# Performance work log

Hardware: AMD Instinct MI355X
Metric: run time of the kernel (lower is better)

## Reference

```python
import jax, jax.numpy as jnp
import numpy as np

B, N, F_IN = 8, 1024, 64
HEADS = 8
D = F_IN  # out_features per head (in_features == out_features)


def setup_inputs() -> dict:
    key = jax.random.key(0)
    ks = jax.random.split(key, 5)
    stdv = 1.0 / np.sqrt(F_IN * HEADS)
    h = jax.random.normal(ks[0], (B, N, F_IN), dtype=jnp.float32)
    adj = jnp.ones((B, N, N), dtype=jnp.float32)  # passed but unused by the module
    W = jax.random.uniform(ks[1], (F_IN, D * HEADS), minval=-stdv, maxval=stdv, dtype=jnp.float32)
    a = jax.random.uniform(ks[2], (2 * D, 1), minval=-stdv, maxval=stdv, dtype=jnp.float32)
    out_W = jax.random.normal(ks[3], (D * HEADS, F_IN), dtype=jnp.float32) / np.sqrt(D * HEADS)
    out_b = jnp.zeros((F_IN,), dtype=jnp.float32)
    return {"h": h, "adj": adj, "W": W, "a": a, "out_W": out_W, "out_b": out_b}


def reference(h, adj, W, a, out_W, out_b):
    Bv, Nv, _ = h.shape
    Dh = W.shape[1] // HEADS
    # Wh: [B, N, H, D]
    Wh = (h @ W).reshape(Bv, Nv, HEADS, Dh)
    # Additive attention decomposed: e[b,i,j,h] = leaky_relu(Wh[b,i,h].a_src + Wh[b,j,h].a_dst)
    a_src = jnp.einsum('bnhd,d->bnh', Wh, a[:Dh, 0])
    a_dst = jnp.einsum('bnhd,d->bnh', Wh, a[Dh:, 0])
    e = jax.nn.leaky_relu(a_src[:, :, None, :] + a_dst[:, None, :, :], negative_slope=0.01)  # [B,N,N,H]
    # Module applies softmax over dim=1 (the first node axis i)
    attn = jax.nn.softmax(e, axis=1)  # [B,N,N,H]
    # h_prime[b,i,h,:] = sum_j attn[b,i,j,h] * Wh[b,j,h,:]
    h_prime = jnp.einsum('bijh,bjhd->bihd', attn, Wh).reshape(Bv, Nv, HEADS * Dh)
    return h_prime @ out_W + out_b
```

## Files before the change

kernel.cpp:

```cpp
#include <hip/hip_runtime.h>


#define B_  8
#define N_  1024
#define H_  8
#define D_  64
#define BH_ 64
#define CH_ 32
#define CL_ 32

__device__ __forceinline__ float bcast_lane(float v, int l) {
  return __int_as_float(__builtin_amdgcn_readlane(__float_as_int(v), l));
}

__global__ __launch_bounds__(256) void k_wh(
    const float* __restrict__ h, const float* __restrict__ W,
    const float* __restrict__ a,
    float* __restrict__ Wh, float* __restrict__ sArr, float* __restrict__ tArr) {
  const int tid = threadIdx.x;
  const int lane = tid & 63;
  const int wid = tid >> 6;
  const int row0 = blockIdx.x * 16;
  const int b = row0 >> 10;

  float hreg[16];
#pragma unroll
  for (int r = 0; r < 16; ++r) hreg[r] = h[(row0 + r) * 64 + lane];
  const float a_s = a[lane];
  const float a_t = a[64 + lane];

  float acc0[16], acc1[16];
#pragma unroll
  for (int r = 0; r < 16; ++r) { acc0[r] = 0.f; acc1[r] = 0.f; }
#pragma unroll 4
  for (int k = 0; k < 64; ++k) {
    const float w0 = W[k * 512 + tid];
    const float w1 = W[k * 512 + tid + 256];
#pragma unroll
    for (int r = 0; r < 16; ++r) {
      const float hv = bcast_lane(hreg[r], k);
      acc0[r] += hv * w0;
      acc1[r] += hv * w1;
    }
  }
  const int hh0 = wid, hh1 = wid + 4;
#pragma unroll
  for (int r = 0; r < 16; ++r) {
    const int n = (row0 + r) & (N_ - 1);
    Wh[((b * H_ + hh0) * N_ + n) * D_ + lane] = acc0[r];
    Wh[((b * H_ + hh1) * N_ + n) * D_ + lane] = acc1[r];
  }
#pragma unroll
  for (int r = 0; r < 16; ++r) {
    const int n = (row0 + r) & (N_ - 1);
    float s0 = acc0[r] * a_s, t0 = acc0[r] * a_t;
    float s1 = acc1[r] * a_s, t1 = acc1[r] * a_t;
#pragma unroll
    for (int m = 32; m > 0; m >>= 1) {
      s0 += __shfl_xor(s0, m); t0 += __shfl_xor(t0, m);
      s1 += __shfl_xor(s1, m); t1 += __shfl_xor(t1, m);
    }
    if (lane == 0) {
      sArr[(b * H_ + hh0) * N_ + n] = s0;
      tArr[(b * H_ + hh0) * N_ + n] = t0;
      sArr[(b * H_ + hh1) * N_ + n] = s1;
      tArr[(b * H_ + hh1) * N_ + n] = t1;
    }
  }
}

__global__ __launch_bounds__(1024) void k_sortinc(
    const float* __restrict__ sArr, const float* __restrict__ tArr,
    const float* __restrict__ Wh,
    int* __restrict__ qrk,
    float* __restrict__ INC1, float* __restrict__ INC2,
    float2* __restrict__ cOff) {
  __shared__ float sL[1024];
  __shared__ float tvL[1024];
  __shared__ int   tiL[1024];
  __shared__ float cum1L[1024], cum001L[1024];
  __shared__ float2 cs12L[CH_ * 64];
  __shared__ float ws1[16], ws2[16];
  const int tid = threadIdx.x;
  const int lane = tid & 63;
  const int wv_ = tid >> 6;
  const int bh = blockIdx.x;

  const float orig_s = sArr[bh * N_ + tid];
  float sv_r = orig_s;
  float tv_r = tArr[bh * N_ + tid];
  int   ti_r = tid;

  for (int size = 2; size <= 1024; size <<= 1) {
    for (int stride = size >> 1; stride > 0; stride >>= 1) {
      const bool up = ((tid & size) == 0);
      const bool lower = ((tid & stride) == 0);
      float psv, ptv; int pti;
      if (stride >= 64) {
        sL[tid] = sv_r; tvL[tid] = tv_r; tiL[tid] = ti_r;
        __syncthreads();
        const int p = tid ^ stride;
        psv = sL[p]; ptv = tvL[p]; pti = tiL[p];
        __syncthreads();
      } else {
        psv = __shfl_xor(sv_r, stride);
        ptv = __shfl_xor(tv_r, stride);
        pti = __shfl_xor(ti_r, stride);
      }
      const bool sameDir = (up == lower);
      const bool pLessS = (psv < sv_r);
      if (pLessS == sameDir) sv_r = psv;
      const bool pLessT = (ptv < tv_r) || (ptv == tv_r && pti < ti_r);
      if (pLessT == sameDir) { tv_r = ptv; ti_r = pti; }
    }
  }
  sL[tid] = sv_r; tvL[tid] = tv_r;

  float c1 = __expf(sv_r), c001 = __expf(0.01f * sv_r);
  {
    float a1 = c1, a2 = c001;
#pragma unroll
    for (int off = 1; off < 64; off <<= 1) {
      const float x1 = __shfl_up(a1, off);
      const float x2 = __shfl_up(a2, off);
      if (lane >= off) { a1 += x1; a2 += x2; }
    }
    if (lane == 63) { ws1[wv_] = a1; ws2[wv_] = a2; }
    __syncthreads();
    float o1 = 0.f, o2 = 0.f;
    for (int ww = 0; ww < 16; ++ww) {
      if (ww < wv_) { o1 += ws1[ww]; o2 += ws2[ww]; }
    }
    c1 = a1 + o1; c001 = a2 + o2;
  }
  cum1L[tid] = c1; cum001L[tid] = c001;
  __syncthreads();
  const float totalHi = cum1L[1023];

  float u_r, v_r;
  {
    const float tj = tv_r;
    const float th = -tj;
    int lo = 0, hi = 1024;
    while (lo < hi) { const int mid = (lo + hi) >> 1; if (sL[mid] <= th) lo = mid + 1; else hi = mid; }
    const float S_lo = (lo > 0) ? cum001L[lo - 1] : 0.f;
    const float S_hi = totalHi - ((lo > 0) ? cum1L[lo - 1] : 0.f);
    const float et = __expf(tj), et001 = __expf(0.01f * tj);
    const float Z = et * S_hi + et001 * S_lo;
    u_r = et / Z; v_r = et001 / Z;
  }

  {
    const float th = -orig_s;
    int lo = 0, hi = 1024;
    while (lo < hi) { const int mid = (lo + hi) >> 1; if (tvL[mid] <= th) lo = mid + 1; else hi = mid; }
    qrk[bh * N_ + tid] = lo;
  }

  const int d = lane;
  const int whb = bh * (N_ * D_);
  const int rbase = bh * N_ + wv_ * 64;
  float r1 = 0.f, r2 = 0.f;
#pragma unroll 8
  for (int k2 = 0; k2 < CL_; ++k2) {
    const int   j  = __builtin_amdgcn_readlane(ti_r, k2);
    const float uu = bcast_lane(u_r, k2);
    const float vv = bcast_lane(v_r, k2);
    const float w  = Wh[whb + j * 64 + d];
    r1 += uu * w; r2 += vv * w;
    INC1[(rbase + k2) * 64 + d] = r1;
    INC2[(rbase + k2) * 64 + d] = r2;
  }
  const float csA1 = r1, csA2 = r2;
  r1 = 0.f; r2 = 0.f;
#pragma unroll 8
  for (int k2 = 0; k2 < CL_; ++k2) {
    const int   j  = __builtin_amdgcn_readlane(ti_r, 32 + k2);
    const float uu = bcast_lane(u_r, 32 + k2);
    const float vv = bcast_lane(v_r, 32 + k2);
    const float w  = Wh[whb + j * 64 + d];
    r1 += uu * w; r2 += vv * w;
    INC1[(rbase + 32 + k2) * 64 + d] = r1;
    INC2[(rbase + 32 + k2) * 64 + d] = r2;
  }
  cs12L[(2 * wv_) * 64 + d]     = make_float2(csA1, csA2);
  cs12L[(2 * wv_ + 1) * 64 + d] = make_float2(r1, r2);
  __syncthreads();

  float o1 = 0.f, o2 = 0.f;
  for (int m = 0; m < 2 * wv_; ++m) {
    const float2 cv = cs12L[m * 64 + d];
    o1 += cv.x; o2 += cv.y;
  }
  const int cbase = bh * 33;
  cOff[(cbase + 2 * wv_) * 64 + d]     = make_float2(o1, o2);
  cOff[(cbase + 2 * wv_ + 1) * 64 + d] = make_float2(o1 + csA1, o2 + csA2);
  if (wv_ == 15)
    cOff[(cbase + 32) * 64 + d] = make_float2(o1 + csA1 + r1, o2 + csA2 + r2);
}

__global__ __launch_bounds__(512) void k_out(
    const float* __restrict__ sArr, const int* __restrict__ qrk,
    const float* __restrict__ INC1, const float* __restrict__ INC2,
    const float2* __restrict__ cOff,
    const float* __restrict__ outW, const float* __restrict__ outb,
    float* __restrict__ out) {
  __shared__ float part[8 * 8 * 64];
  __shared__ int   rkI[16 * 8];
  __shared__ float esL[16 * 8], es001L[16 * 8];
  const int tid = threadIdx.x;
  const int row0 = blockIdx.x * 16;
  const int b = row0 >> 10;
  const int p = tid >> 6;
  const int lane = tid & 63;

  if (tid < 128) {
    const int r = tid >> 3, hh = tid & 7;
    const int bh = b * H_ + hh;
    const int n = (row0 + r) & (N_ - 1);
    const float si = sArr[bh * N_ + n];
    rkI[tid] = qrk[bh * N_ + n];
    esL[tid] = __expf(si);
    es001L[tid] = __expf(0.01f * si);
  }
  __syncthreads();

  float hpv[16];
  {
    const int bh = b * H_ + p;
    const int cbase = bh * 33;
    const float T1 = cOff[(cbase + 32) * 64 + lane].x;
#pragma unroll
    for (int r = 0; r < 16; ++r) {
      const int rk = rkI[r * 8 + p];
      float i1 = 0.f, i2 = 0.f;
      if (rk > 0) {
        const int idx = rk - 1, cc = idx >> 5;
        const float2 co = cOff[(cbase + cc) * 64 + lane];
        i1 = INC1[(bh * N_ + idx) * 64 + lane] + co.x;
        i2 = INC2[(bh * N_ + idx) * 64 + lane] + co.y;
      }
      hpv[r] = esL[r * 8 + p] * (T1 - i1) + es001L[r * 8 + p] * i2;
    }
  }

  float acc[16];
#pragma unroll
  for (int r = 0; r < 16; ++r) acc[r] = 0.f;
#pragma unroll 4
  for (int kc = 0; kc < 64; ++kc) {
    const float wvv = outW[(p * 64 + kc) * 64 + lane];
#pragma unroll
    for (int r = 0; r < 16; ++r) {
      const float hv = bcast_lane(hpv[r], kc);
      acc[r] += hv * wvv;
    }
  }

  for (int half = 0; half < 2; ++half) {
#pragma unroll
    for (int r = 0; r < 8; ++r) part[(p * 8 + r) * 64 + lane] = acc[half * 8 + r];
    __syncthreads();
    {
      const int r2 = tid >> 6, c2 = tid & 63;
      float ssum = 0.f;
#pragma unroll
      for (int p2 = 0; p2 < 8; ++p2) ssum += part[(p2 * 8 + r2) * 64 + c2];
      out[(row0 + half * 8 + r2) * 64 + c2] = outb[c2] + ssum;
    }
    __syncthreads();
  }
}

extern "C" void kernel_launch(void* const* d_in, const int* in_sizes, int n_in,
                              void* d_out, int out_size, void* d_ws, size_t ws_size,
                              hipStream_t stream) {
  const float* h    = (const float*)d_in[0];
  const float* W    = (const float*)d_in[2];
  const float* a    = (const float*)d_in[3];
  const float* outW = (const float*)d_in[4];
  const float* outb = (const float*)d_in[5];
  float* out = (float*)d_out;

  float* ws   = (float*)d_ws;
  float* Wh   = ws;
  float* sArr = Wh + (size_t)BH_ * N_ * D_;
  float* tArr = sArr + BH_ * N_;
  int*   qrk  = (int*)(tArr + BH_ * N_);
  float* INC1 = (float*)(qrk + BH_ * N_);
  float* INC2 = INC1 + (size_t)BH_ * N_ * D_;
  float2* cOff = (float2*)(INC2 + (size_t)BH_ * N_ * D_);

  hipLaunchKernelGGL(k_wh,      dim3((B_ * N_) / 16), dim3(256), 0, stream,
                     h, W, a, Wh, sArr, tArr);
  hipLaunchKernelGGL(k_sortinc, dim3(BH_), dim3(1024), 0, stream,
                     sArr, tArr, Wh, qrk, INC1, INC2, cOff);
  hipLaunchKernelGGL(k_out,     dim3((B_ * N_) / 16), dim3(512), 0, stream,
                     sArr, qrk, INC1, INC2, cOff, outW, outb, out);
}
```

Baseline: 160.8 us.

## Fuse three kernels into one persistent kernel with grid-wide barriers

Merges the Wh projection, the sort/prefix stage and the output projection into a single 256-block persistent kernel, using atomic-counter grid barriers between phases. The incremental prefix-sum work is now spread across all blocks (8 waves per block, one 32-element chunk each) instead of only 64 blocks, and chunk offsets are computed in a separate phase. This removes launch gaps and underutilisation of the sort stage, but adds barrier spin costs, a memset, and extra global round-trips for u/v/index arrays. It relies on all 256 blocks of 1024 threads being co-resident to avoid deadlock.

New measurement: 250.8 us. +55.9%, slower.

```diff
diff --git a/kernel.cpp b/kernel.cpp
--- a/kernel.cpp
+++ b/kernel.cpp
@@ -13,262 +13,263 @@
   return __int_as_float(__builtin_amdgcn_readlane(__float_as_int(v), l));
 }
 
-__global__ __launch_bounds__(256) void k_wh(
+__device__ __forceinline__ void gridbar(unsigned int* cnt, unsigned int target) {
+  __syncthreads();
+  if (threadIdx.x == 0) {
+    __threadfence();
+    __hip_atomic_fetch_add(cnt, 1u, __ATOMIC_RELEASE, __HIP_MEMORY_SCOPE_AGENT);
+    while (__hip_atomic_load(cnt, __ATOMIC_ACQUIRE, __HIP_MEMORY_SCOPE_AGENT) < target)
+      __builtin_amdgcn_s_sleep(1);
+    __threadfence();
+  }
+  __syncthreads();
+}
+
+__global__ __launch_bounds__(1024) void k_fused(
     const float* __restrict__ h, const float* __restrict__ W,
     const float* __restrict__ a,
-    float* __restrict__ Wh, float* __restrict__ sArr, float* __restrict__ tArr) {
-  const int tid = threadIdx.x;
-  const int lane = tid & 63;
-  const int wid = tid >> 6;
-  const int row0 = blockIdx.x * 16;
-  const int b = row0 >> 10;
-
-  float hreg[16];
-#pragma unroll
-  for (int r = 0; r < 16; ++r) hreg[r] = h[(row0 + r) * 64 + lane];
-  const float a_s = a[lane];
-  const float a_t = a[64 + lane];
-
-  float acc0[16], acc1[16];
-#pragma unroll
-  for (int r = 0; r < 16; ++r) { acc0[r] = 0.f; acc1[r] = 0.f; }
-#pragma unroll 4
-  for (int k = 0; k < 64; ++k) {
-    const float w0 = W[k * 512 + tid];
-    const float w1 = W[k * 512 + tid + 256];
-#pragma unroll
-    for (int r = 0; r < 16; ++r) {
-      const float hv = bcast_lane(hreg[r], k);
-      acc0[r] += hv * w0;
-      acc1[r] += hv * w1;
-    }
-  }
-  const int hh0 = wid, hh1 = wid + 4;
-#pragma unroll
-  for (int r = 0; r < 16; ++r) {
-    const int n = (row0 + r) & (N_ - 1);
-    Wh[((b * H_ + hh0) * N_ + n) * D_ + lane] = acc0[r];
-    Wh[((b * H_ + hh1) * N_ + n) * D_ + lane] = acc1[r];
-  }
-#pragma unroll
-  for (int r = 0; r < 16; ++r) {
-    const int n = (row0 + r) & (N_ - 1);
-    float s0 = acc0[r] * a_s, t0 = acc0[r] * a_t;
-    float s1 = acc1[r] * a_s, t1 = acc1[r] * a_t;
-#pragma unroll
-    for (int m = 32; m > 0; m >>= 1) {
-      s0 += __shfl_xor(s0, m); t0 += __shfl_xor(t0, m);
-      s1 += __shfl_xor(s1, m); t1 += __shfl_xor(t1, m);
-    }
-    if (lane == 0) {
-      sArr[(b * H_ + hh0) * N_ + n] = s0;
-      tArr[(b * H_ + hh0) * N_ + n] = t0;
-      sArr[(b * H_ + hh1) * N_ + n] = s1;
-      tArr[(b * H_ + hh1) * N_ + n] = t1;
-    }
-  }
-}
-
-__global__ __launch_bounds__(1024) void k_sortinc(
-    const float* __restrict__ sArr, const float* __restrict__ tArr,
-    const float* __restrict__ Wh,
+    const float* __restrict__ outW, const float* __restrict__ outb,
+    float* __restrict__ out,
+    float* __restrict__ Wh, float* __restrict__ sArr, float* __restrict__ tArr,
+    int* __restrict__ tsi, float* __restrict__ uArr, float* __restrict__ vArr,
     int* __restrict__ qrk,
     float* __restrict__ INC1, float* __restrict__ INC2,
-    float2* __restrict__ cOff) {
+    float2* __restrict__ csG, float2* __restrict__ cOff,
+    unsigned int* __restrict__ bar) {
   __shared__ float sL[1024];
   __shared__ float tvL[1024];
   __shared__ int   tiL[1024];
   __shared__ float cum1L[1024], cum001L[1024];
-  __shared__ float2 cs12L[CH_ * 64];
   __shared__ float ws1[16], ws2[16];
+  __shared__ float part[2 * 8 * 8 * 64];
+  __shared__ int   rkI[32 * 8];
+  __shared__ float esL[32 * 8], es001L[32 * 8];
+
   const int tid = threadIdx.x;
   const int lane = tid & 63;
-  const int wv_ = tid >> 6;
-  const int bh = blockIdx.x;
-
-  const float orig_s = sArr[bh * N_ + tid];
-  float sv_r = orig_s;
-  float tv_r = tArr[bh * N_ + tid];
-  int   ti_r = tid;
-
-  for (int size = 2; size <= 1024; size <<= 1) {
-    for (int stride = size >> 1; stride > 0; stride >>= 1) {
-      const bool up = ((tid & size) == 0);
-      const bool lower = ((tid & stride) == 0);
-      float psv, ptv; int pti;
-      if (stride >= 64) {
-        sL[tid] = sv_r; tvL[tid] = tv_r; tiL[tid] = ti_r;
-        __syncthreads();
-        const int p = tid ^ stride;
-        psv = sL[p]; ptv = tvL[p]; pti = tiL[p];
-        __syncthreads();
-      } else {
-        psv = __shfl_xor(sv_r, stride);
-        ptv = __shfl_xor(tv_r, stride);
-        pti = __shfl_xor(ti_r, stride);
-      }
-      const bool sameDir = (up == lower);
-      const bool pLessS = (psv < sv_r);
-      if (pLessS == sameDir) sv_r = psv;
-      const bool pLessT = (ptv < tv_r) || (ptv == tv_r && pti < ti_r);
-      if (pLessT == sameDir) { tv_r = ptv; ti_r = pti; }
-    }
-  }
-  sL[tid] = sv_r; tvL[tid] = tv_r;
-
-  float c1 = __expf(sv_r), c001 = __expf(0.01f * sv_r);
+  const int wv = tid >> 6;
+  const int bi = blockIdx.x;
+
   {
-    float a1 = c1, a2 = c001;
-#pragma unroll
-    for (int off = 1; off < 64; off <<= 1) {
-      const float x1 = __shfl_up(a1, off);
-      const float x2 = __shfl_up(a2, off);
-      if (lane >= off) { a1 += x1; a2 += x2; }
-    }
-    if (lane == 63) { ws1[wv_] = a1; ws2[wv_] = a2; }
+    const int g = wv >> 2, w2 = wv & 3;
+    const int row0 = bi * 32 + g * 8;
+    const int b = row0 >> 10;
+    float hreg[8];
+#pragma unroll
+    for (int r = 0; r < 8; ++r) hreg[r] = h[(row0 + r) * 64 + lane];
+    const float a_s = a[lane];
+    const float a_t = a[64 + lane];
+
+    float acc0[8], acc1[8];
+#pragma unroll
+    for (int r = 0; r < 8; ++r) { acc0[r] = 0.f; acc1[r] = 0.f; }
+#pragma unroll 4
+    for (int k = 0; k < 64; ++k) {
+      const float w0 = W[k * 512 + w2 * 64 + lane];
+      const float w1 = W[k * 512 + 256 + w2 * 64 + lane];
+#pragma unroll
+      for (int r = 0; r < 8; ++r) {
+        const float hv = bcast_lane(hreg[r], k);
+        acc0[r] += hv * w0;
+        acc1[r] += hv * w1;
+      }
+    }
+    const int hh0 = w2, hh1 = w2 + 4;
+#pragma unroll
+    for (int r = 0; r < 8; ++r) {
+      const int n = (row0 + r) & (N_ - 1);
+      Wh[((b * H_ + hh0) * N_ + n) * D_ + lane] = acc0[r];
+      Wh[((b * H_ + hh1) * N_ + n) * D_ + lane] = acc1[r];
+    }
+#pragma unroll
+    for (int r = 0; r < 8; ++r) {
+      const int n = (row0 + r) & (N_ - 1);
+      float s0 = acc0[r] * a_s, t0 = acc0[r] * a_t;
+      float s1 = acc1[r] * a_s, t1 = acc1[r] * a_t;
+#pragma unroll
+      for (int m = 32; m > 0; m >>= 1) {
+        s0 += __shfl_xor(s0, m); t0 += __shfl_xor(t0, m);
+        s1 += __shfl_xor(s1, m); t1 += __shfl_xor(t1, m);
+      }
+      if (lane == 0) {
+        sArr[(b * H_ + hh0) * N_ + n] = s0;
+        tArr[(b * H_ + hh0) * N_ + n] = t0;
+        sArr[(b * H_ + hh1) * N_ + n] = s1;
+        tArr[(b * H_ + hh1) * N_ + n] = t1;
+      }
+    }
+  }
+  gridbar(bar, 256);
+
+  if (bi < BH_) {
+    const int bh = bi;
+    const float orig_s = sArr[bh * N_ + tid];
+    float sv_r = orig_s;
+    float tv_r = tArr[bh * N_ + tid];
+    int   ti_r = tid;
+
+    for (int size = 2; size <= 1024; size <<= 1) {
+      for (int stride = size >> 1; stride > 0; stride >>= 1) {
+        const bool up = ((tid & size) == 0);
+        const bool lower = ((tid & stride) == 0);
+        float psv, ptv; int pti;
+        if (stride >= 64) {
+          sL[tid] = sv_r; tvL[tid] = tv_r; tiL[tid] = ti_r;
+          __syncthreads();
+          const int p = tid ^ stride;
+          psv = sL[p]; ptv = tvL[p]; pti = tiL[p];
+          __syncthreads();
+        } else {
+          psv = __shfl_xor(sv_r, stride);
+          ptv = __shfl_xor(tv_r, stride);
+          pti = __shfl_xor(ti_r, stride);
+        }
+        const bool sameDir = (up == lower);
+        const bool pLessS = (psv < sv_r);
+        if (pLessS == sameDir) sv_r = psv;
+        const bool pLessT = (ptv < tv_r) || (ptv == tv_r && pti < ti_r);
+        if (pLessT == sameDir) { tv_r = ptv; ti_r = pti; }
+      }
+    }
+    sL[tid] = sv_r; tvL[tid] = tv_r;
+
+    float c1 = __expf(sv_r), c001 = __expf(0.01f * sv_r);
+    {
+      float a1 = c1, a2 = c001;
+#pragma unroll
+      for (int off = 1; off < 64; off <<= 1) {
+        const float x1 = __shfl_up(a1, off);
+        const float x2 = __shfl_up(a2, off);
+        if (lane >= off) { a1 += x1; a2 += x2; }
+      }
+      if (lane == 63) { ws1[wv] = a1; ws2[wv] = a2; }
+      __syncthreads();
+      float o1 = 0.f, o2 = 0.f;
+      for (int ww = 0; ww < 16; ++ww) {
+        if (ww < wv) { o1 += ws1[ww]; o2 += ws2[ww]; }
+      }
+      c1 = a1 + o1; c001 = a2 + o2;
+    }
+    cum1L[tid] = c1; cum001L[tid] = c001;
     __syncthreads();
+    const float totalHi = cum1L[1023];
+
+    {
+      const float tj = tv_r;
+      const float th = -tj;
+      int lo = 0, hi = 1024;
+      while (lo < hi) { const int mid = (lo + hi) >> 1; if (sL[mid] <= th) lo = mid + 1; else hi = mid; }
+      const float S_lo = (lo > 0) ? cum001L[lo - 1] : 0.f;
+      const float S_hi = totalHi - ((lo > 0) ? cum1L[lo - 1] : 0.f);
+      const float et = __expf(tj), et001 = __expf(0.01f * tj);
+      const float Z = et * S_hi + et001 * S_lo;
+      uArr[bh * N_ + tid] = et / Z;
+      vArr[bh * N_ + tid] = et001 / Z;
+      tsi[bh * N_ + tid] = ti_r;
+    }
+    {
+      const float th = -orig_s;
+      int lo = 0, hi = 1024;
+      while (lo < hi) { const int mid = (lo + hi) >> 1; if (tvL[mid] <= th) lo = mid + 1; else hi = mid; }
+      qrk[bh * N_ + tid] = lo;
+    }
+  }
+  gridbar(bar, 512);
+
+  if (wv < 8) {
+    const int id = bi * 8 + wv;
+    const int bh = id >> 5, c = id & (CH_ - 1);
+    const int rb = bh * N_ + c * CL_;
+    int jv = 0; float uv = 0.f, vvx = 0.f;
+    if (lane < 32) {
+      jv  = tsi[rb + lane];
+      uv  = uArr[rb + lane];
+      vvx = vArr[rb + lane];
+    }
+    const int whb = bh * (N_ * D_);
+    float r1 = 0.f, r2 = 0.f;
+#pragma unroll 8
+    for (int k2 = 0; k2 < CL_; ++k2) {
+      const int   j  = __builtin_amdgcn_readlane(jv, k2);
+      const float uu = bcast_lane(uv, k2);
+      const float vv2 = bcast_lane(vvx, k2);
+      const float w = Wh[whb + j * 64 + lane];
+      r1 += uu * w; r2 += vv2 * w;
+      INC1[(rb + k2) * 64 + lane] = r1;
+      INC2[(rb + k2) * 64 + lane] = r2;
+    }
+    csG[(bh * CH_ + c) * 64 + lane] = make_float2(r1, r2);
+  }
+  gridbar(bar, 768);
+
+  if (bi < BH_ && wv == 0) {
+    const int cb = bi * 33;
     float o1 = 0.f, o2 = 0.f;
-    for (int ww = 0; ww < 16; ++ww) {
-      if (ww < wv_) { o1 += ws1[ww]; o2 += ws2[ww]; }
-    }
-    c1 = a1 + o1; c001 = a2 + o2;
-  }
-  cum1L[tid] = c1; cum001L[tid] = c001;
-  __syncthreads();
-  const float totalHi = cum1L[1023];
-
-  float u_r, v_r;
+    for (int m = 0; m < CH_; ++m) {
+      const float2 cv = csG[(bi * CH_ + m) * 64 + lane];
+      cOff[(cb + m) * 64 + lane] = make_float2(o1, o2);
+      o1 += cv.x; o2 += cv.y;
+    }
+    cOff[(cb + 32) * 64 + lane] = make_float2(o1, o2);
+  }
+  gridbar(bar, 1024);
+
   {
-    const float tj = tv_r;
-    const float th = -tj;
-    int lo = 0, hi = 1024;
-    while (lo < hi) { const int mid = (lo + hi) >> 1; if (sL[mid] <= th) lo = mid + 1; else hi = mid; }
-    const float S_lo = (lo > 0) ? cum001L[lo - 1] : 0.f;
-    const float S_hi = totalHi - ((lo > 0) ? cum1L[lo - 1] : 0.f);
-    const float et = __expf(tj), et001 = __expf(0.01f * tj);
-    const float Z = et * S_hi + et001 * S_lo;
-    u_r = et / Z; v_r = et001 / Z;
-  }
-
-  {
-    const float th = -orig_s;
-    int lo = 0, hi = 1024;
-    while (lo < hi) { const int mid = (lo + hi) >> 1; if (tvL[mid] <= th) lo = mid + 1; else hi = mid; }
-    qrk[bh * N_ + tid] = lo;
-  }
-
-  const int d = lane;
-  const int whb = bh * (N_ * D_);
-  const int rbase = bh * N_ + wv_ * 64;
-  float r1 = 0.f, r2 = 0.f;
-#pragma unroll 8
-  for (int k2 = 0; k2 < CL_; ++k2) {
-    const int   j  = __builtin_amdgcn_readlane(ti_r, k2);
-    const float uu = bcast_lane(u_r, k2);
-    const float vv = bcast_lane(v_r, k2);
-    const float w  = Wh[whb + j * 64 + d];
-    r1 += uu * w; r2 += vv * w;
-    INC1[(rbase + k2) * 64 + d] = r1;
-    INC2[(rbase + k2) * 64 + d] = r2;
-  }
-  const float csA1 = r1, csA2 = r2;
-  r1 = 0.f; r2 = 0.f;
-#pragma unroll 8
-  for (int k2 = 0; k2 < CL_; ++k2) {
-    const int   j  = __builtin_amdgcn_readlane(ti_r, 32 + k2);
-    const float uu = bcast_lane(u_r, 32 + k2);
-    const float vv = bcast_lane(v_r, 32 + k2);
-    const float w  = Wh[whb + j * 64 + d];
-    r1 += uu * w; r2 += vv * w;
-    INC1[(rbase + 32 + k2) * 64 + d] = r1;
-    INC2[(rbase + 32 + k2) * 64 + d] = r2;
-  }
-  cs12L[(2 * wv_) * 64 + d]     = make_float2(csA1, csA2);
-  cs12L[(2 * wv_ + 1) * 64 + d] = make_float2(r1, r2);
-  __syncthreads();
-
-  float o1 = 0.f, o2 = 0.f;
-  for (int m = 0; m < 2 * wv_; ++m) {
-    const float2 cv = cs12L[m * 64 + d];
-    o1 += cv.x; o2 += cv.y;
-  }
-  const int cbase = bh * 33;
-  cOff[(cbase + 2 * wv_) * 64 + d]     = make_float2(o1, o2);
-  cOff[(cbase + 2 * wv_ + 1) * 64 + d] = make_float2(o1 + csA1, o2 + csA2);
-  if (wv_ == 15)
-    cOff[(cbase + 32) * 64 + d] = make_float2(o1 + csA1 + r1, o2 + csA2 + r2);
-}
-
-__global__ __launch_bounds__(512) void k_out(
-    const float* __restrict__ sArr, const int* __restrict__ qrk,
-    const float* __restrict__ INC1, const float* __restrict__ INC2,
-    const float2* __restrict__ cOff,
-    const float* __restrict__ outW, const float* __restrict__ outb,
-    float* __restrict__ out) {
-  __shared__ float part[8 * 8 * 64];
-  __shared__ int   rkI[16 * 8];
-  __shared__ float esL[16 * 8], es001L[16 * 8];
-  const int tid = threadIdx.x;
-  const int row0 = blockIdx.x * 16;
-  const int b = row0 >> 10;
-  const int p = tid >> 6;
-  const int lane = tid & 63;
-
-  if (tid < 128) {
-    const int r = tid >> 3, hh = tid & 7;
-    const int bh = b * H_ + hh;
-    const int n = (row0 + r) & (N_ - 1);
-    const float si = sArr[bh * N_ + n];
-    rkI[tid] = qrk[bh * N_ + n];
-    esL[tid] = __expf(si);
-    es001L[tid] = __expf(0.01f * si);
-  }
-  __syncthreads();
-
-  float hpv[16];
-  {
+    const int hb = wv >> 3, p = wv & 7;
+    const int row0 = bi * 32;
+    const int b = row0 >> 10;
+    if (tid < 256) {
+      const int r = tid >> 3, hh = tid & 7;
+      const int bh = b * H_ + hh;
+      const int n = (row0 + r) & (N_ - 1);
+      const float si = sArr[bh * N_ + n];
+      rkI[tid] = qrk[bh * N_ + n];
+      esL[tid] = __expf(si);
+      es001L[tid] = __expf(0.01f * si);
+    }
+    __syncthreads();
+
     const int bh = b * H_ + p;
-    const int cbase = bh * 33;
-    const float T1 = cOff[(cbase + 32) * 64 + lane].x;
+    const int cb = bh * 33;
+    const float T1 = cOff[(cb + 32) * 64 + lane].x;
+    float hpv[16];
 #pragma unroll
     for (int r = 0; r < 16; ++r) {
-      const int rk = rkI[r * 8 + p];
+      const int rr = hb * 16 + r;
+      const int rk = rkI[rr * 8 + p];
       float i1 = 0.f, i2 = 0.f;
       if (rk > 0) {
         const int idx = rk - 1, cc = idx >> 5;
-        const float2 co = cOff[(cbase + cc) * 64 + lane];
+        const float2 co = cOff[(cb + cc) * 64 + lane];
         i1 = INC1[(bh * N_ + idx) * 64 + lane] + co.x;
         i2 = INC2[(bh * N_ + idx) * 64 + lane] + co.y;
       }
-      hpv[r] = esL[r * 8 + p] * (T1 - i1) + es001L[r * 8 + p] * i2;
-    }
-  }
-
-  float acc[16];
-#pragma unroll
-  for (int r = 0; r < 16; ++r) acc[r] = 0.f;
+      hpv[r] = esL[rr * 8 + p] * (T1 - i1) + es001L[rr * 8 + p] * i2;
+    }
+
+    float acc[16];
+#pragma unroll
+    for (int r = 0; r < 16; ++r) acc[r] = 0.f;
 #pragma unroll 4
-  for (int kc = 0; kc < 64; ++kc) {
-    const float wvv = outW[(p * 64 + kc) * 64 + lane];
-#pragma unroll
-    for (int r = 0; r < 16; ++r) {
-      const float hv = bcast_lane(hpv[r], kc);
-      acc[r] += hv * wvv;
-    }
-  }
-
-  for (int half = 0; half < 2; ++half) {
-#pragma unroll
-    for (int r = 0; r < 8; ++r) part[(p * 8 + r) * 64 + lane] = acc[half * 8 + r];
-    __syncthreads();
-    {
-      const int r2 = tid >> 6, c2 = tid & 63;
-      float ssum = 0.f;
-#pragma unroll
-      for (int p2 = 0; p2 < 8; ++p2) ssum += part[(p2 * 8 + r2) * 64 + c2];
-      out[(row0 + half * 8 + r2) * 64 + c2] = outb[c2] + ssum;
-    }
-    __syncthreads();
+    for (int kc = 0; kc < 64; ++kc) {
+      const float wvv = outW[(p * 64 + kc) * 64 + lane];
+#pragma unroll
+      for (int r = 0; r < 16; ++r) acc[r] += bcast_lane(hpv[r], kc) * wvv;
+    }
+
+    float* pp = part + hb * (8 * 8 * 64);
+    for (int half = 0; half < 2; ++half) {
+#pragma unroll
+      for (int r = 0; r < 8; ++r) pp[(p * 8 + r) * 64 + lane] = acc[half * 8 + r];
+      __syncthreads();
+      {
+        float ssum = 0.f;
+#pragma unroll
+        for (int p2 = 0; p2 < 8; ++p2) ssum += pp[(p2 * 8 + p) * 64 + lane];
+        out[(row0 + hb * 16 + half * 8 + p) * 64 + lane] = outb[lane] + ssum;
+      }
+      __syncthreads();
+    }
   }
 }
 
@@ -286,15 +287,19 @@
   float* Wh   = ws;
   float* sArr = Wh + (size_t)BH_ * N_ * D_;
   float* tArr = sArr + BH_ * N_;
-  int*   qrk  = (int*)(tArr + BH_ * N_);
-  float* INC1 = (float*)(qrk + BH_ * N_);
+  float* uArr = tArr + BH_ * N_;
+  float* vArr = uArr + BH_ * N_;
+  float* INC1 = vArr + BH_ * N_;
   float* INC2 = INC1 + (size_t)BH_ * N_ * D_;
-  float2* cOff = (float2*)(INC2 + (size_t)BH_ * N_ * D_);
-
-  hipLaunchKernelGGL(k_wh,      dim3((B_ * N_) / 16), dim3(256), 0, stream,
-                     h, W, a, Wh, sArr, tArr);
-  hipLaunchKernelGGL(k_sortinc, dim3(BH_), dim3(1024), 0, stream,
-                     sArr, tArr, Wh, qrk, INC1, INC2, cOff);
-  hipLaunchKernelGGL(k_out,     dim3((B_ * N_) / 16), dim3(512), 0, stream,
-                     sArr, qrk, INC1, INC2, cOff, outW, outb, out);
+  int*   tsi  = (int*)(INC2 + (size_t)BH_ * N_ * D_);
+  int*   qrk  = tsi + BH_ * N_;
+  float2* csG  = (float2*)(qrk + BH_ * N_);
+  float2* cOff = csG + (size_t)BH_ * CH_ * 64;
+  unsigned int* bar = (unsigned int*)(cOff + (size_t)BH_ * 33 * 64);
+
+  hipMemsetAsync(bar, 0, sizeof(unsigned int), stream);
+  hipLaunchKernelGGL(k_fused, dim3(256), dim3(1024), 0, stream,
+                     h, W, a, outW, outb, out,
+                     Wh, sArr, tArr, tsi, uArr, vArr, qrk,
+                     INC1, INC2, csG, cOff, bar);
 }
```

## Fuse sort/prefix kernel with output projection, recompute partial sums on-chip

Applied to the files above, without the earlier changes.

Merges the sort/prefix-sum kernel and the output-projection kernel into one kernel of 256 blocks, four per batch-head, each handling a quarter of the rows. It no longer writes the full INC1/INC2 prefix arrays to global memory. Each block keeps 16-element chunk sums in LDS and recomputes the within-chunk partial sum per row from Wh. Per-head output projections are combined with atomicAdd into a zeroed output. This removes large global traffic and one launch, but repeats the bitonic sort four times per batch-head and adds a memset plus float atomics.

Result: slower. 204.5 us (+27.2%).

```diff
diff --git a/kernel.cpp b/kernel.cpp
--- a/kernel.cpp
+++ b/kernel.cpp
@@ -6,8 +6,6 @@
 #define H_  8
 #define D_  64
 #define BH_ 64
-#define CH_ 32
-#define CL_ 32
 
 __device__ __forceinline__ float bcast_lane(float v, int l) {
   return __int_as_float(__builtin_amdgcn_readlane(__float_as_int(v), l));
@@ -69,22 +67,29 @@
   }
 }
 
-__global__ __launch_bounds__(1024) void k_sortinc(
+__global__ __launch_bounds__(1024) void k_rest(
     const float* __restrict__ sArr, const float* __restrict__ tArr,
     const float* __restrict__ Wh,
-    int* __restrict__ qrk,
-    float* __restrict__ INC1, float* __restrict__ INC2,
-    float2* __restrict__ cOff) {
-  __shared__ float sL[1024];
-  __shared__ float tvL[1024];
+    const float* __restrict__ outW, const float* __restrict__ outb,
+    float* __restrict__ out) {
+  __shared__ float2 uni[65 * 64];
+  float* sL      = (float*)uni;
+  float* tvL     = sL + 1024;
+  float* cum1L   = tvL + 1024;
+  float* cum001L = cum1L + 1024;
+  float2* csOff  = uni;
   __shared__ int   tiL[1024];
-  __shared__ float cum1L[1024], cum001L[1024];
-  __shared__ float2 cs12L[CH_ * 64];
+  __shared__ float uL[1024], vL[1024];
+  __shared__ int   rkL[1024];
+  __shared__ float esL[1024], es001L[1024];
   __shared__ float ws1[16], ws2[16];
+
   const int tid = threadIdx.x;
   const int lane = tid & 63;
-  const int wv_ = tid >> 6;
-  const int bh = blockIdx.x;
+  const int wv = tid >> 6;
+  const int bi = blockIdx.x;
+  const int bh = bi >> 2, q = bi & 3;
+  const int b = bh >> 3, hh = bh & 7;
 
   const float orig_s = sArr[bh * N_ + tid];
   float sv_r = orig_s;
@@ -114,7 +119,7 @@
       if (pLessT == sameDir) { tv_r = ptv; ti_r = pti; }
     }
   }
-  sL[tid] = sv_r; tvL[tid] = tv_r;
+  sL[tid] = sv_r; tvL[tid] = tv_r; tiL[tid] = ti_r;
 
   float c1 = __expf(sv_r), c001 = __expf(0.01f * sv_r);
   {
@@ -125,11 +130,11 @@
       const float x2 = __shfl_up(a2, off);
       if (lane >= off) { a1 += x1; a2 += x2; }
     }
-    if (lane == 63) { ws1[wv_] = a1; ws2[wv_] = a2; }
+    if (lane == 63) { ws1[wv] = a1; ws2[wv] = a2; }
     __syncthreads();
     float o1 = 0.f, o2 = 0.f;
     for (int ww = 0; ww < 16; ++ww) {
-      if (ww < wv_) { o1 += ws1[ww]; o2 += ws2[ww]; }
+      if (ww < wv) { o1 += ws1[ww]; o2 += ws2[ww]; }
     }
     c1 = a1 + o1; c001 = a2 + o2;
   }
@@ -148,128 +153,97 @@
     const float et = __expf(tj), et001 = __expf(0.01f * tj);
     const float Z = et * S_hi + et001 * S_lo;
     u_r = et / Z; v_r = et001 / Z;
-  }
-
+    uL[tid] = u_r; vL[tid] = v_r;
+  }
   {
     const float th = -orig_s;
     int lo = 0, hi = 1024;
     while (lo < hi) { const int mid = (lo + hi) >> 1; if (tvL[mid] <= th) lo = mid + 1; else hi = mid; }
-    qrk[bh * N_ + tid] = lo;
-  }
-
-  const int d = lane;
+    rkL[tid] = lo;
+    esL[tid] = __expf(orig_s);
+    es001L[tid] = __expf(0.01f * orig_s);
+  }
+  __syncthreads();
+
   const int whb = bh * (N_ * D_);
-  const int rbase = bh * N_ + wv_ * 64;
-  float r1 = 0.f, r2 = 0.f;
+  {
+    float r1 = 0.f, r2 = 0.f;
 #pragma unroll 8
-  for (int k2 = 0; k2 < CL_; ++k2) {
-    const int   j  = __builtin_amdgcn_readlane(ti_r, k2);
-    const float uu = bcast_lane(u_r, k2);
-    const float vv = bcast_lane(v_r, k2);
-    const float w  = Wh[whb + j * 64 + d];
-    r1 += uu * w; r2 += vv * w;
-    INC1[(rbase + k2) * 64 + d] = r1;
-    INC2[(rbase + k2) * 64 + d] = r2;
-  }
-  const float csA1 = r1, csA2 = r2;
-  r1 = 0.f; r2 = 0.f;
-#pragma unroll 8
-  for (int k2 = 0; k2 < CL_; ++k2) {
-    const int   j  = __builtin_amdgcn_readlane(ti_r, 32 + k2);
-    const float uu = bcast_lane(u_r, 32 + k2);
-    const float vv = bcast_lane(v_r, 32 + k2);
-    const float w  = Wh[whb + j * 64 + d];
-    r1 += uu * w; r2 += vv * w;
-    INC1[(rbase + 32 + k2) * 64 + d] = r1;
-    INC2[(rbase + 32 + k2) * 64 + d] = r2;
-  }
-  cs12L[(2 * wv_) * 64 + d]     = make_float2(csA1, csA2);
-  cs12L[(2 * wv_ + 1) * 64 + d] = make_float2(r1, r2);
-  __syncthreads();
-
-  float o1 = 0.f, o2 = 0.f;
-  for (int m = 0; m < 2 * wv_; ++m) {
-    const float2 cv = cs12L[m * 64 + d];
-    o1 += cv.x; o2 += cv.y;
-  }
-  const int cbase = bh * 33;
-  cOff[(cbase + 2 * wv_) * 64 + d]     = make_float2(o1, o2);
-  cOff[(cbase + 2 * wv_ + 1) * 64 + d] = make_float2(o1 + csA1, o2 + csA2);
-  if (wv_ == 15)
-    cOff[(cbase + 32) * 64 + d] = make_float2(o1 + csA1 + r1, o2 + csA2 + r2);
-}
-
-__global__ __launch_bounds__(512) void k_out(
-    const float* __restrict__ sArr, const int* __restrict__ qrk,
-    const float* __restrict__ INC1, const float* __restrict__ INC2,
-    const float2* __restrict__ cOff,
-    const float* __restrict__ outW, const float* __restrict__ outb,
-    float* __restrict__ out) {
-  __shared__ float part[8 * 8 * 64];
-  __shared__ int   rkI[16 * 8];
-  __shared__ float esL[16 * 8], es001L[16 * 8];
-  const int tid = threadIdx.x;
-  const int row0 = blockIdx.x * 16;
-  const int b = row0 >> 10;
-  const int p = tid >> 6;
-  const int lane = tid & 63;
-
-  if (tid < 128) {
-    const int r = tid >> 3, hh = tid & 7;
-    const int bh = b * H_ + hh;
-    const int n = (row0 + r) & (N_ - 1);
-    const float si = sArr[bh * N_ + n];
-    rkI[tid] = qrk[bh * N_ + n];
-    esL[tid] = __expf(si);
-    es001L[tid] = __expf(0.01f * si);
-  }
-  __syncthreads();
-
+    for (int k2 = 0; k2 < 64; ++k2) {
+      const int   j  = __builtin_amdgcn_readlane(ti_r, k2);
+      const float uu = bcast_lane(u_r, k2);
+      const float vv = bcast_lane(v_r, k2);
+      const float w  = Wh[whb + j * 64 + lane];
+      r1 += uu * w; r2 += vv * w;
+      if ((k2 & 15) == 15) {
+        csOff[(4 * wv + (k2 >> 4) + 1) * 64 + lane] = make_float2(r1, r2);
+        r1 = 0.f; r2 = 0.f;
+      }
+    }
+  }
+  if (tid < 64) csOff[tid] = make_float2(0.f, 0.f);
+  __syncthreads();
+
+  float2 off[4];
+  float2 tot = make_float2(0.f, 0.f);
+  {
+#pragma unroll
+    for (int cc = 0; cc < 4; ++cc) {
+      const int c = wv * 4 + cc;
+      float o1 = 0.f, o2 = 0.f;
+      for (int m = 1; m <= c; ++m) {
+        const float2 cv = csOff[m * 64 + lane];
+        o1 += cv.x; o2 += cv.y;
+      }
+      off[cc] = make_float2(o1, o2);
+      if (c == 63) {
+        const float2 last = csOff[64 * 64 + lane];
+        tot = make_float2(o1 + last.x, o2 + last.y);
+      }
+    }
+  }
+  __syncthreads();
+#pragma unroll
+  for (int cc = 0; cc < 4; ++cc)
+    csOff[(wv * 4 + cc) * 64 + lane] = off[cc];
+  if (wv == 15) csOff[64 * 64 + lane] = tot;
+  __syncthreads();
+
+  const int rbase = q * 256 + wv * 16;
+  const float T1 = csOff[64 * 64 + lane].x;
   float hpv[16];
-  {
-    const int bh = b * H_ + p;
-    const int cbase = bh * 33;
-    const float T1 = cOff[(cbase + 32) * 64 + lane].x;
-#pragma unroll
-    for (int r = 0; r < 16; ++r) {
-      const int rk = rkI[r * 8 + p];
-      float i1 = 0.f, i2 = 0.f;
-      if (rk > 0) {
-        const int idx = rk - 1, cc = idx >> 5;
-        const float2 co = cOff[(cbase + cc) * 64 + lane];
-        i1 = INC1[(bh * N_ + idx) * 64 + lane] + co.x;
-        i2 = INC2[(bh * N_ + idx) * 64 + lane] + co.y;
-      }
-      hpv[r] = esL[r * 8 + p] * (T1 - i1) + es001L[r * 8 + p] * i2;
-    }
+#pragma unroll 2
+  for (int r = 0; r < 16; ++r) {
+    const int i = rbase + r;
+    const int rk = rkL[i];
+    float i1 = 0.f, i2 = 0.f;
+    if (rk > 0) {
+      const int idx = rk - 1, c = idx >> 4;
+      const float2 co = csOff[c * 64 + lane];
+      i1 = co.x; i2 = co.y;
+      for (int k = c * 16; k <= idx; ++k) {
+        const int j = tiL[k];
+        const float w = Wh[whb + j * 64 + lane];
+        i1 += uL[k] * w;
+        i2 += vL[k] * w;
+      }
+    }
+    hpv[r] = esL[i] * (T1 - i1) + es001L[i] * i2;
   }
 
   float acc[16];
-#pragma unroll
-  for (int r = 0; r < 16; ++r) acc[r] = 0.f;
+  const float binit = (hh == 0) ? outb[lane] : 0.f;
+#pragma unroll
+  for (int r = 0; r < 16; ++r) acc[r] = binit;
 #pragma unroll 4
   for (int kc = 0; kc < 64; ++kc) {
-    const float wvv = outW[(p * 64 + kc) * 64 + lane];
-#pragma unroll
-    for (int r = 0; r < 16; ++r) {
-      const float hv = bcast_lane(hpv[r], kc);
-      acc[r] += hv * wvv;
-    }
-  }
-
-  for (int half = 0; half < 2; ++half) {
-#pragma unroll
-    for (int r = 0; r < 8; ++r) part[(p * 8 + r) * 64 + lane] = acc[half * 8 + r];
-    __syncthreads();
-    {
-      const int r2 = tid >> 6, c2 = tid & 63;
-      float ssum = 0.f;
-#pragma unroll
-      for (int p2 = 0; p2 < 8; ++p2) ssum += part[(p2 * 8 + r2) * 64 + c2];
-      out[(row0 + half * 8 + r2) * 64 + c2] = outb[c2] + ssum;
-    }
-    __syncthreads();
-  }
+    const float wvv = outW[(hh * 64 + kc) * 64 + lane];
+#pragma unroll
+    for (int r = 0; r < 16; ++r) acc[r] += bcast_lane(hpv[r], kc) * wvv;
+  }
+#pragma unroll
+  for (int r = 0; r < 16; ++r)
+    atomicAdd(&out[(b * N_ + rbase + r) * 64 + lane], acc[r]);
 }
 
 extern "C" void kernel_launch(void* const* d_in, const int* in_sizes, int n_in,
@@ -286,15 +260,10 @@
   float* Wh   = ws;
   float* sArr = Wh + (size_t)BH_ * N_ * D_;
   float* tArr = sArr + BH_ * N_;
-  int*   qrk  = (int*)(tArr + BH_ * N_);
-  float* INC1 = (float*)(qrk + BH_ * N_);
-  float* INC2 = INC1 + (size_t)BH_ * N_ * D_;
-  float2* cOff = (float2*)(INC2 + (size_t)BH_ * N_ * D_);
-
-  hipLaunchKernelGGL(k_wh,      dim3((B_ * N_) / 16), dim3(256), 0, stream,
+
+  hipMemsetAsync(out, 0, (size_t)B_ * N_ * 64 * sizeof(float), stream);
+  hipLaunchKernelGGL(k_wh,   dim3((B_ * N_) / 16), dim3(256), 0, stream,
                      h, W, a, Wh, sArr, tArr);
-  hipLaunchKernelGGL(k_sortinc, dim3(BH_), dim3(1024), 0, stream,
-                     sArr, tArr, Wh, qrk, INC1, INC2, cOff);
-  hipLaunchKernelGGL(k_out,     dim3((B_ * N_) / 16), dim3(512), 0, stream,
-                     sArr, qrk, INC1, INC2, cOff, outW, outb, out);
-}
+  hipLaunchKernelGGL(k_rest, dim3(BH_ * 4), dim3(1024), 0, stream,
+                     sArr, tArr, Wh, outW, outb, out);
+}
```

## Split inclusive prefix-sum writes into separate wide kernel with chunk offsets

Applied to the files above, without the earlier changes.

The sort kernel (64 blocks) now computes only per-chunk sums and offsets, saving the sorted indices and u/v weights to global memory. A new kernel with 2048 small blocks recomputes the within-chunk running sums, starting from the chunk offset, and writes a single interleaved float2 INC array. This moves the large write traffic off the 64-block launch and spreads it across the whole GPU. k_out now does one float2 load with no separate offset add. In exchange there is an extra launch, the Wh gathers are read twice, and the index/uv arrays make an extra global round trip.

Result: no change. 158.8 us (-1.2%).

```diff
diff --git a/kernel.cpp b/kernel.cpp
--- a/kernel.cpp
+++ b/kernel.cpp
@@ -69,17 +69,16 @@
   }
 }
 
-__global__ __launch_bounds__(1024) void k_sortinc(
+__global__ __launch_bounds__(1024) void k_sort(
     const float* __restrict__ sArr, const float* __restrict__ tArr,
     const float* __restrict__ Wh,
-    int* __restrict__ qrk,
-    float* __restrict__ INC1, float* __restrict__ INC2,
-    float2* __restrict__ cOff) {
+    int* __restrict__ tsi, float2* __restrict__ uvArr,
+    int* __restrict__ qrk, float2* __restrict__ cOff) {
   __shared__ float sL[1024];
   __shared__ float tvL[1024];
   __shared__ int   tiL[1024];
   __shared__ float cum1L[1024], cum001L[1024];
-  __shared__ float2 cs12L[CH_ * 64];
+  __shared__ float2 wsT[16 * 64];
   __shared__ float ws1[16], ws2[16];
   const int tid = threadIdx.x;
   const int lane = tid & 63;
@@ -148,8 +147,9 @@
     const float et = __expf(tj), et001 = __expf(0.01f * tj);
     const float Z = et * S_hi + et001 * S_lo;
     u_r = et / Z; v_r = et001 / Z;
-  }
-
+    uvArr[bh * N_ + tid] = make_float2(u_r, v_r);
+    tsi[bh * N_ + tid] = ti_r;
+  }
   {
     const float th = -orig_s;
     int lo = 0, hi = 1024;
@@ -157,52 +157,60 @@
     qrk[bh * N_ + tid] = lo;
   }
 
-  const int d = lane;
   const int whb = bh * (N_ * D_);
-  const int rbase = bh * N_ + wv_ * 64;
-  float r1 = 0.f, r2 = 0.f;
+  float r1a = 0.f, r2a = 0.f, r1b = 0.f, r2b = 0.f;
 #pragma unroll 8
   for (int k2 = 0; k2 < CL_; ++k2) {
-    const int   j  = __builtin_amdgcn_readlane(ti_r, k2);
-    const float uu = bcast_lane(u_r, k2);
-    const float vv = bcast_lane(v_r, k2);
-    const float w  = Wh[whb + j * 64 + d];
-    r1 += uu * w; r2 += vv * w;
-    INC1[(rbase + k2) * 64 + d] = r1;
-    INC2[(rbase + k2) * 64 + d] = r2;
-  }
-  const float csA1 = r1, csA2 = r2;
-  r1 = 0.f; r2 = 0.f;
+    const int   ja = __builtin_amdgcn_readlane(ti_r, k2);
+    const float ua = bcast_lane(u_r, k2);
+    const float va = bcast_lane(v_r, k2);
+    const int   jb = __builtin_amdgcn_readlane(ti_r, 32 + k2);
+    const float ub = bcast_lane(u_r, 32 + k2);
+    const float vb = bcast_lane(v_r, 32 + k2);
+    const float wa = Wh[whb + ja * 64 + lane];
+    const float wb = Wh[whb + jb * 64 + lane];
+    r1a += ua * wa; r2a += va * wa;
+    r1b += ub * wb; r2b += vb * wb;
+  }
+  wsT[wv_ * 64 + lane] = make_float2(r1a + r1b, r2a + r2b);
+  __syncthreads();
+  float o1 = 0.f, o2 = 0.f;
+  for (int ww = 0; ww < 16; ++ww) {
+    if (ww < wv_) { const float2 t = wsT[ww * 64 + lane]; o1 += t.x; o2 += t.y; }
+  }
+  const int cb = bh * 33;
+  cOff[(cb + 2 * wv_) * 64 + lane]     = make_float2(o1, o2);
+  cOff[(cb + 2 * wv_ + 1) * 64 + lane] = make_float2(o1 + r1a, o2 + r2a);
+  if (wv_ == 15)
+    cOff[(cb + 32) * 64 + lane] = make_float2(o1 + r1a + r1b, o2 + r2a + r2b);
+}
+
+__global__ __launch_bounds__(64) void k_inc(
+    const float* __restrict__ Wh, const int* __restrict__ tsi,
+    const float2* __restrict__ uvArr, const float2* __restrict__ cOff,
+    float2* __restrict__ INC12) {
+  const int blk = blockIdx.x;
+  const int bh = ((blk >> 8) << 3) | (blk & 7);
+  const int c  = (blk >> 3) & 31;
+  const int d = threadIdx.x;
+  const float2 off = cOff[(bh * 33 + c) * 64 + d];
+  float r1 = off.x, r2 = off.y;
+  const int base = bh * N_ + c * CL_;
+  const int whb = bh * (N_ * D_);
 #pragma unroll 8
   for (int k2 = 0; k2 < CL_; ++k2) {
-    const int   j  = __builtin_amdgcn_readlane(ti_r, 32 + k2);
-    const float uu = bcast_lane(u_r, 32 + k2);
-    const float vv = bcast_lane(v_r, 32 + k2);
-    const float w  = Wh[whb + j * 64 + d];
-    r1 += uu * w; r2 += vv * w;
-    INC1[(rbase + 32 + k2) * 64 + d] = r1;
-    INC2[(rbase + 32 + k2) * 64 + d] = r2;
-  }
-  cs12L[(2 * wv_) * 64 + d]     = make_float2(csA1, csA2);
-  cs12L[(2 * wv_ + 1) * 64 + d] = make_float2(r1, r2);
-  __syncthreads();
-
-  float o1 = 0.f, o2 = 0.f;
-  for (int m = 0; m < 2 * wv_; ++m) {
-    const float2 cv = cs12L[m * 64 + d];
-    o1 += cv.x; o2 += cv.y;
-  }
-  const int cbase = bh * 33;
-  cOff[(cbase + 2 * wv_) * 64 + d]     = make_float2(o1, o2);
-  cOff[(cbase + 2 * wv_ + 1) * 64 + d] = make_float2(o1 + csA1, o2 + csA2);
-  if (wv_ == 15)
-    cOff[(cbase + 32) * 64 + d] = make_float2(o1 + csA1 + r1, o2 + csA2 + r2);
+    const int j = tsi[base + k2];
+    const float2 uv = uvArr[base + k2];
+    const float w = Wh[whb + j * 64 + d];
+    r1 += uv.x * w;
+    r2 += uv.y * w;
+    INC12[(base + k2) * 64 + d] = make_float2(r1, r2);
+  }
 }
 
 __global__ __launch_bounds__(512) void k_out(
     const float* __restrict__ sArr, const int* __restrict__ qrk,
-    const float* __restrict__ INC1, const float* __restrict__ INC2,
-    const float2* __restrict__ cOff,
+    const float2* __restrict__ INC12, const float2* __restrict__ cOff,
     const float* __restrict__ outW, const float* __restrict__ outb,
     float* __restrict__ out) {
   __shared__ float part[8 * 8 * 64];
@@ -228,17 +236,14 @@
   float hpv[16];
   {
     const int bh = b * H_ + p;
-    const int cbase = bh * 33;
-    const float T1 = cOff[(cbase + 32) * 64 + lane].x;
+    const float T1 = cOff[(bh * 33 + 32) * 64 + lane].x;
 #pragma unroll
     for (int r = 0; r < 16; ++r) {
       const int rk = rkI[r * 8 + p];
       float i1 = 0.f, i2 = 0.f;
       if (rk > 0) {
-        const int idx = rk - 1, cc = idx >> 5;
-        const float2 co = cOff[(cbase + cc) * 64 + lane];
-        i1 = INC1[(bh * N_ + idx) * 64 + lane] + co.x;
-        i2 = INC2[(bh * N_ + idx) * 64 + lane] + co.y;
+        const float2 I = INC12[(bh * N_ + rk - 1) * 64 + lane];
+        i1 = I.x; i2 = I.y;
       }
       hpv[r] = esL[r * 8 + p] * (T1 - i1) + es001L[r * 8 + p] * i2;
     }
@@ -286,15 +291,18 @@
   float* Wh   = ws;
   float* sArr = Wh + (size_t)BH_ * N_ * D_;
   float* tArr = sArr + BH_ * N_;
-  int*   qrk  = (int*)(tArr + BH_ * N_);
-  float* INC1 = (float*)(qrk + BH_ * N_);
-  float* INC2 = INC1 + (size_t)BH_ * N_ * D_;
-  float2* cOff = (float2*)(INC2 + (size_t)BH_ * N_ * D_);
-
-  hipLaunchKernelGGL(k_wh,      dim3((B_ * N_) / 16), dim3(256), 0, stream,
+  int*   tsi  = (int*)(tArr + BH_ * N_);
+  int*   qrk  = tsi + BH_ * N_;
+  float2* uvArr = (float2*)(qrk + BH_ * N_);
+  float2* cOff  = uvArr + (size_t)BH_ * N_;
+  float2* INC12 = cOff + (size_t)BH_ * 33 * 64;
+
+  hipLaunchKernelGGL(k_wh,   dim3((B_ * N_) / 16), dim3(256), 0, stream,
                      h, W, a, Wh, sArr, tArr);
-  hipLaunchKernelGGL(k_sortinc, dim3(BH_), dim3(1024), 0, stream,
-                     sArr, tArr, Wh, qrk, INC1, INC2, cOff);
-  hipLaunchKernelGGL(k_out,     dim3((B_ * N_) / 16), dim3(512), 0, stream,
-                     sArr, qrk, INC1, INC2, cOff, outW, outb, out);
-}
+  hipLaunchKernelGGL(k_sort, dim3(BH_), dim3(1024), 0, stream,
+                     sArr, tArr, Wh, tsi, uvArr, qrk, cOff);
+  hipLaunchKernelGGL(k_inc,  dim3(BH_ * CH_), dim3(64), 0, stream,
+                     Wh, tsi, uvArr, cOff, INC12);
+  hipLaunchKernelGGL(k_out,  dim3((B_ * N_) / 16), dim3(512), 0, stream,
+                     sArr, qrk, INC12, cOff, outW, outb, out);
+}
```
